# Kernel tuning notes

Measured on AMD Instinct MI355X. Metric: run time of the kernel, lower is better.

The kernel has to match this reference:

```python
import jax, jax.numpy as jnp
import numpy as np

N_NODES = 100000
IN_CH = 256
OUT_CH = 64
N_EDGES = 3200000


def setup_inputs() -> dict:
    key = jax.random.key(0)
    k1, k2, k3, k4 = jax.random.split(key, 4)
    x = jax.random.normal(k1, (N_NODES, IN_CH), dtype=jnp.float32)
    edge_index = jax.random.randint(k2, (2, N_EDGES), 0, N_NODES, dtype=jnp.int64)
    # GCNConv parameters (glorot-style init for W, zeros for bias as in PyG)
    W = jax.random.normal(k3, (IN_CH, OUT_CH), dtype=jnp.float32) / np.sqrt(IN_CH)
    b = jnp.zeros((OUT_CH,), dtype=jnp.float32)
    return {"x": x, "edge_index": edge_index, "W": W, "b": b}


def reference(x, edge_index, W, b):
    N = x.shape[0]
    # --- GCNConv: add self-loops, symmetric degree normalization ---
    loops = jnp.arange(N, dtype=edge_index.dtype)
    src = jnp.concatenate([edge_index[0], loops])  # [E+N]
    dst = jnp.concatenate([edge_index[1], loops])  # [E+N]
    # degree of each target node (edge weights = 1)
    deg = jax.ops.segment_sum(jnp.ones_like(dst, dtype=x.dtype), dst, num_segments=N)
    dinv = jnp.where(deg > 0, jax.lax.rsqrt(deg), 0.0)  # deg^{-1/2}
    norm = dinv[src] * dinv[dst]                        # [E+N]
    # linear transform first (PyG applies lin before propagate)
    h = x @ W                                           # [N, OUT_CH]
    msg = h[src] * norm[:, None]                        # gather + scale
    out = jax.ops.segment_sum(msg, dst, num_segments=N) + b  # scatter-add + bias
    # --- relu + log_softmax ---
    out = jax.nn.relu(out)
    return jax.nn.log_softmax(out, axis=-1)
```

## Files before the change

kernel.cpp:

```cpp
#include <hip/hip_runtime.h>
#include <cstddef>
#include <cstdint>

#define N_NODES 100000
#define IN_CH 256
#define OUT_CH 64
#define N_EDGES 3200000

#define BKT_SHIFT 7
#define BKT_R     128
#define K_BKT     782
#define T_PART    8192
#define NBLK_PART ((N_EDGES + T_PART - 1) / T_PART)

#define WS_FLAG_OFF   0
#define WS_BBASE_OFF  3264
#define WS_BTOT_OFF   6400
#define WS_DINV_OFF   9600
#define WS_NOFF_OFF   409600
#define WS_PAIRS_OFF  809728
#define WS_SSRC_OFF   13609728
#define WS_H_OFF      26409728
#define WS_NEED       39209728

#define WSF_DEG_OFF   4096
#define WSF_DINV_OFF  404096
#define WSF_H_OFF     804096

typedef __attribute__((ext_vector_type(8))) short bshort8;
typedef __attribute__((ext_vector_type(4))) float f32x4;
typedef __attribute__((ext_vector_type(4))) unsigned u32x4;

static __device__ __forceinline__ unsigned short f2bf(float f) {
    unsigned u = __builtin_bit_cast(unsigned, f);
    u += 0x7FFFu + ((u >> 16) & 1u);
    return (unsigned short)(u >> 16);
}
static __device__ __forceinline__ float bflo(unsigned u) {
    return __builtin_bit_cast(float, u << 16);
}
static __device__ __forceinline__ float bfhi(unsigned u) {
    return __builtin_bit_cast(float, u & 0xFFFF0000u);
}

__global__ void probe_kernel(const unsigned* __restrict__ ei, int* __restrict__ flag) {
    if (blockIdx.x == 0 && threadIdx.x == 0) {
        int all0 = 1;
        for (int i = 0; i < 16; ++i) all0 &= (ei[2 * i + 1] == 0u);
        *flag = all0;
    }
}

__device__ __forceinline__ int load_idx(const int* ei32, const long long* ei64,
                                        bool is64, long long pos) {
    return is64 ? (int)ei64[pos] : ei32[pos];
}

__global__ __launch_bounds__(256) void bcount_kernel(const int* __restrict__ ei32,
                                                     const long long* __restrict__ ei64,
                                                     const int* __restrict__ flag,
                                                     unsigned* __restrict__ hist2d) {
    __shared__ unsigned hist[K_BKT];
    const bool is64 = (*flag != 0);
    const int start = blockIdx.x * T_PART;
    const int end   = min(start + T_PART, N_EDGES);
    for (int k = threadIdx.x; k < K_BKT; k += 256) hist[k] = 0u;
    __syncthreads();
    if (is64) {
        const longlong2* d2 = (const longlong2*)&ei64[N_EDGES];
        for (int i = (start >> 1) + threadIdx.x; i < (end >> 1); i += 256) {
            longlong2 d = d2[i];
            atomicAdd(&hist[(int)d.x >> BKT_SHIFT], 1u);
            atomicAdd(&hist[(int)d.y >> BKT_SHIFT], 1u);
        }
    } else {
        const int2* d2 = (const int2*)&ei32[N_EDGES];
        for (int i = (start >> 1) + threadIdx.x; i < (end >> 1); i += 256) {
            int2 d = d2[i];
            atomicAdd(&hist[d.x >> BKT_SHIFT], 1u);
            atomicAdd(&hist[d.y >> BKT_SHIFT], 1u);
        }
    }
    __syncthreads();
    for (int k = threadIdx.x; k < K_BKT; k += 256)
        hist2d[(size_t)blockIdx.x * K_BKT + k] = hist[k];
}

__global__ __launch_bounds__(256) void bscanA_kernel(const unsigned* __restrict__ hist2d,
                                                     unsigned* __restrict__ btot) {
    const int k = blockIdx.x * 4 + (threadIdx.x >> 6);
    const int lane = threadIdx.x & 63;
    if (k >= K_BKT) return;
    unsigned tot = 0u;
    for (int c = lane; c < NBLK_PART; c += 64)
        tot += hist2d[(size_t)c * K_BKT + k];
    #pragma unroll
    for (int o = 32; o; o >>= 1) tot += __shfl_xor(tot, o);
    if (lane == 0) btot[k] = tot;
}

__global__ __launch_bounds__(1024) void bscanB_kernel(const unsigned* __restrict__ btot,
                                                      unsigned* __restrict__ bbase,
                                                      unsigned* __restrict__ noff) {
    __shared__ unsigned s[1024];
    const int t = threadIdx.x;
    unsigned v = (t < K_BKT) ? btot[t] : 0u;
    s[t] = v; __syncthreads();
    #pragma unroll
    for (int d = 1; d < 1024; d <<= 1) {
        unsigned x = (t >= d) ? s[t - d] : 0u; __syncthreads();
        s[t] += x; __syncthreads();
    }
    if (t < K_BKT) {
        bbase[t] = s[t] - v;
        if (t == K_BKT - 1) bbase[K_BKT] = s[t];
    }
    if (t == 0) noff[N_NODES] = N_EDGES;
}

__global__ __launch_bounds__(256) void bscanC_kernel(unsigned* __restrict__ hist2d,
                                                     const unsigned* __restrict__ bbase) {
    const int k = blockIdx.x * 4 + (threadIdx.x >> 6);
    const int lane = threadIdx.x & 63;
    if (k >= K_BKT) return;
    unsigned run = bbase[k];
    for (int c0 = 0; c0 < NBLK_PART; c0 += 64) {
        int blk = c0 + lane;
        unsigned v = (blk < NBLK_PART) ? hist2d[(size_t)blk * K_BKT + k] : 0u;
        unsigned incl = v;
        #pragma unroll
        for (int d = 1; d < 64; d <<= 1) {
            unsigned tq = __shfl_up(incl, d);
            if (lane >= d) incl += tq;
        }
        if (blk < NBLK_PART) hist2d[(size_t)blk * K_BKT + k] = run + incl - v;
        run += __shfl(incl, 63);
    }
}

__global__ __launch_bounds__(512) void partition_kernel(const int* __restrict__ ei32,
                                                        const long long* __restrict__ ei64,
                                                        const int* __restrict__ flag,
                                                        const unsigned* __restrict__ hist2d,
                                                        unsigned* __restrict__ pairs) {
    __shared__ unsigned cur[K_BKT];
    const bool is64 = (*flag != 0);
    const int start = blockIdx.x * T_PART;
    const int end   = min(start + T_PART, N_EDGES);
    for (int k = threadIdx.x; k < K_BKT; k += 512)
        cur[k] = hist2d[(size_t)blockIdx.x * K_BKT + k];
    __syncthreads();
    if (is64) {
        const longlong2* s2 = (const longlong2*)&ei64[0];
        const longlong2* d2 = (const longlong2*)&ei64[N_EDGES];
        for (int i = (start >> 1) + threadIdx.x; i < (end >> 1); i += 512) {
            longlong2 s = s2[i];
            longlong2 d = d2[i];
            unsigned p0 = atomicAdd(&cur[(int)d.x >> BKT_SHIFT], 1u);
            pairs[p0] = (unsigned)s.x | ((unsigned)((int)d.x & (BKT_R - 1)) << 17);
            unsigned p1 = atomicAdd(&cur[(int)d.y >> BKT_SHIFT], 1u);
            pairs[p1] = (unsigned)s.y | ((unsigned)((int)d.y & (BKT_R - 1)) << 17);
        }
    } else {
        const int2* s2 = (const int2*)&ei32[0];
        const int2* d2 = (const int2*)&ei32[N_EDGES];
        for (int i = (start >> 1) + threadIdx.x; i < (end >> 1); i += 512) {
            int2 s = s2[i];
            int2 d = d2[i];
            unsigned p0 = atomicAdd(&cur[d.x >> BKT_SHIFT], 1u);
            pairs[p0] = (unsigned)s.x | ((unsigned)(d.x & (BKT_R - 1)) << 17);
            unsigned p1 = atomicAdd(&cur[d.y >> BKT_SHIFT], 1u);
            pairs[p1] = (unsigned)s.y | ((unsigned)(d.y & (BKT_R - 1)) << 17);
        }
    }
}

__global__ __launch_bounds__(256) void sort2_kernel(const unsigned* __restrict__ pairs,
                                                    const unsigned* __restrict__ bbase,
                                                    int* __restrict__ ssrc,
                                                    unsigned* __restrict__ noff,
                                                    float* __restrict__ dinv) {
    __shared__ unsigned hist[BKT_R];
    __shared__ unsigned cur[BKT_R];
    const int k = blockIdx.x;
    const int t = threadIdx.x;
    const unsigned segS = bbase[k], segE = bbase[k + 1];

    if (t < BKT_R) hist[t] = 0u;
    __syncthreads();
    for (unsigned j = segS + t; j < segE; j += 256)
        atomicAdd(&hist[pairs[j] >> 17], 1u);
    __syncthreads();
    if (t < BKT_R) cur[t] = hist[t];
    __syncthreads();
    #pragma unroll
    for (int d = 1; d < BKT_R; d <<= 1) {
        unsigned x = (t < BKT_R && t >= d) ? cur[t - d] : 0u;
        __syncthreads();
        if (t < BKT_R) cur[t] += x;
        __syncthreads();
    }
    if (t < BKT_R) {
        unsigned mydeg = hist[t];
        unsigned start = segS + cur[t] - mydeg;
        int n = k * BKT_R + t;
        if (n < N_NODES) {
            noff[n] = start;
            dinv[n] = rsqrtf((float)(mydeg + 1u));
        }
        cur[t] = start;
    }
    __syncthreads();
    for (unsigned j = segS + t; j < segE; j += 256) {
        unsigned p = pairs[j];
        unsigned pos = atomicAdd(&cur[p >> 17], 1u);
        ssrc[pos] = (int)(p & 0x1FFFF);
    }
}

__global__ __launch_bounds__(256) void gemm_kernel(const float* __restrict__ x,
                                                   const float* __restrict__ W,
                                                   const float* __restrict__ dinv,
                                                   unsigned short* __restrict__ hs) {
    __shared__ unsigned short Wf[8][4][64][8];
    const int tid = threadIdx.x;
    const int lane = tid & 63;
    const int wv = tid >> 6;

    for (int i = tid; i < 8 * 4 * 64 * 8; i += 256) {
        int kt = i >> 11;
        int rem = i & 2047;
        int ct = rem >> 9;
        int rem2 = rem & 511;
        int l = rem2 >> 3;
        int j = rem2 & 7;
        int kk = kt * 32 + (l >> 4) * 8 + j;
        int cc = ct * 16 + (l & 15);
        ((unsigned short*)Wf)[i] = f2bf(W[(size_t)kk * OUT_CH + cc]);
    }
    __syncthreads();

    const int r16 = lane & 15;
    const int q = lane >> 4;

    for (int t = blockIdx.x * 4 + wv; t < N_NODES / 16; t += gridDim.x * 4) {
        const int row0 = t * 16;
        const float* xrow = &x[(size_t)(row0 + r16) * IN_CH + q * 8];
        f32x4 acc[4] = {{0.f,0.f,0.f,0.f},{0.f,0.f,0.f,0.f},
                        {0.f,0.f,0.f,0.f},{0.f,0.f,0.f,0.f}};
        #pragma unroll
        for (int kt = 0; kt < 8; ++kt) {
            float4 x0 = *(const float4*)&xrow[kt * 32];
            float4 x1 = *(const float4*)&xrow[kt * 32 + 4];
            unsigned p0, p1, p2, p3;
            asm("v_cvt_pk_bf16_f32 %0, %1, %2" : "=v"(p0) : "v"(x0.x), "v"(x0.y));
            asm("v_cvt_pk_bf16_f32 %0, %1, %2" : "=v"(p1) : "v"(x0.z), "v"(x0.w));
            asm("v_cvt_pk_bf16_f32 %0, %1, %2" : "=v"(p2) : "v"(x1.x), "v"(x1.y));
            asm("v_cvt_pk_bf16_f32 %0, %1, %2" : "=v"(p3) : "v"(x1.z), "v"(x1.w));
            u32x4 au = {p0, p1, p2, p3};
            bshort8 af = __builtin_bit_cast(bshort8, au);
            #pragma unroll
            for (int ct = 0; ct < 4; ++ct) {
                bshort8 bf = *(const bshort8*)&Wf[kt][ct][lane][0];
                acc[ct] = __builtin_amdgcn_mfma_f32_16x16x32_bf16(af, bf, acc[ct], 0, 0, 0);
            }
        }
        float dv[4];
        #pragma unroll
        for (int r = 0; r < 4; ++r) dv[r] = dinv[row0 + q * 4 + r];
        #pragma unroll
        for (int ct = 0; ct < 4; ++ct) {
            #pragma unroll
            for (int r = 0; r < 4; ++r) {
                int row = row0 + q * 4 + r;
                hs[(size_t)row * OUT_CH + ct * 16 + r16] = f2bf(acc[ct][r] * dv[r]);
            }
        }
    }
}

__global__ __launch_bounds__(256) void reduce_kernel(const unsigned short* __restrict__ hs,
                                                     const float* __restrict__ dinv,
                                                     const unsigned* __restrict__ noff,
                                                     const int* __restrict__ ssrc,
                                                     const float* __restrict__ b,
                                                     float* __restrict__ out) {
    const int n = blockIdx.x * 4 + (threadIdx.x >> 6);
    const int lane = threadIdx.x & 63;
    const int q = lane >> 4;
    const int l16 = lane & 15;
    if (n >= N_NODES) return;
    const uint2* h8 = (const uint2*)hs;
    float a0 = 0.f, a1 = 0.f, a2 = 0.f, a3 = 0.f;
    {
        uint2 sv = h8[(size_t)n * 16 + l16];
        if (q == 0) { a0 = bflo(sv.x); a1 = bfhi(sv.x); a2 = bflo(sv.y); a3 = bfhi(sv.y); }
    }
    unsigned j = noff[n];
    const unsigned end = noff[n + 1];
    for (; j + 16 <= end; j += 16) {
        int s0 = ssrc[j + q];
        int s1 = ssrc[j + 4 + q];
        int s2 = ssrc[j + 8 + q];
        int s3 = ssrc[j + 12 + q];
        uint2 v0 = h8[(size_t)s0 * 16 + l16];
        uint2 v1 = h8[(size_t)s1 * 16 + l16];
        uint2 v2 = h8[(size_t)s2 * 16 + l16];
        uint2 v3 = h8[(size_t)s3 * 16 + l16];
        a0 += bflo(v0.x); a1 += bfhi(v0.x); a2 += bflo(v0.y); a3 += bfhi(v0.y);
        a0 += bflo(v1.x); a1 += bfhi(v1.x); a2 += bflo(v1.y); a3 += bfhi(v1.y);
        a0 += bflo(v2.x); a1 += bfhi(v2.x); a2 += bflo(v2.y); a3 += bfhi(v2.y);
        a0 += bflo(v3.x); a1 += bfhi(v3.x); a2 += bflo(v3.y); a3 += bfhi(v3.y);
    }
    for (; j + 4 <= end; j += 4) {
        int s = ssrc[j + q];
        uint2 v = h8[(size_t)s * 16 + l16];
        a0 += bflo(v.x); a1 += bfhi(v.x); a2 += bflo(v.y); a3 += bfhi(v.y);
    }
    unsigned rem = end - j;
    if ((unsigned)q < rem) {
        int s = ssrc[j + q];
        uint2 v = h8[(size_t)s * 16 + l16];
        a0 += bflo(v.x); a1 += bfhi(v.x); a2 += bflo(v.y); a3 += bfhi(v.y);
    }
    a0 += __shfl_xor(a0, 16); a0 += __shfl_xor(a0, 32);
    a1 += __shfl_xor(a1, 16); a1 += __shfl_xor(a1, 32);
    a2 += __shfl_xor(a2, 16); a2 += __shfl_xor(a2, 32);
    a3 += __shfl_xor(a3, 16); a3 += __shfl_xor(a3, 32);
    const float dn = dinv[n];
    float4 bb = ((const float4*)b)[l16];
    float v0 = fmaxf(fmaf(a0, dn, bb.x), 0.f);
    float v1 = fmaxf(fmaf(a1, dn, bb.y), 0.f);
    float v2 = fmaxf(fmaf(a2, dn, bb.z), 0.f);
    float v3 = fmaxf(fmaf(a3, dn, bb.w), 0.f);
    float m = fmaxf(fmaxf(v0, v1), fmaxf(v2, v3));
    #pragma unroll
    for (int o = 8; o; o >>= 1) m = fmaxf(m, __shfl_xor(m, o));
    float sum = expf(v0 - m) + expf(v1 - m) + expf(v2 - m) + expf(v3 - m);
    #pragma unroll
    for (int o = 8; o; o >>= 1) sum += __shfl_xor(sum, o);
    float ls = logf(sum);
    if (q == 0) {
        float4 r;
        r.x = (v0 - m) - ls; r.y = (v1 - m) - ls;
        r.z = (v2 - m) - ls; r.w = (v3 - m) - ls;
        *(float4*)&out[(size_t)n * OUT_CH + l16 * 4] = r;
    }
}

__global__ __launch_bounds__(256) void deg_kernel(const int* __restrict__ ei32,
                                                  const long long* __restrict__ ei64,
                                                  const int* __restrict__ flag,
                                                  unsigned* __restrict__ deg) {
    const bool is64 = (*flag != 0);
    int i = blockIdx.x * blockDim.x + threadIdx.x;
    const int stride = gridDim.x * blockDim.x;
    for (; i < N_EDGES; i += stride) {
        int d = load_idx(ei32, ei64, is64, (long long)N_EDGES + i);
        atomicAdd(&deg[d], 1u);
    }
}

__global__ __launch_bounds__(256) void dinv_kernel(const unsigned* __restrict__ deg,
                                                   float* __restrict__ dinv) {
    int i = blockIdx.x * blockDim.x + threadIdx.x;
    if (i < N_NODES) dinv[i] = rsqrtf((float)(deg[i] + 1u));
}

__global__ __launch_bounds__(256) void scatter_kernel(const int* __restrict__ ei32,
                                                      const long long* __restrict__ ei64,
                                                      const int* __restrict__ flag,
                                                      const unsigned short* __restrict__ hs,
                                                      const float* __restrict__ dinv,
                                                      float* __restrict__ out) {
    const bool is64 = (*flag != 0);
    const int lane = threadIdx.x & 63;
    int w = blockIdx.x * (blockDim.x >> 6) + (threadIdx.x >> 6);
    const int nw = gridDim.x * (blockDim.x >> 6);
    for (int e = w; e < N_EDGES; e += nw) {
        int s = load_idx(ei32, ei64, is64, e);
        int d = load_idx(ei32, ei64, is64, (long long)N_EDGES + e);
        unsigned short us = hs[(size_t)s * OUT_CH + lane];
        float hv = __builtin_bit_cast(float, (unsigned)us << 16);
        atomicAdd(&out[(size_t)d * OUT_CH + lane], hv * dinv[d]);
    }
}

__global__ __launch_bounds__(256) void final_kernel(const unsigned short* __restrict__ hs,
                                                    const float* __restrict__ dinv,
                                                    const float* __restrict__ b,
                                                    float* __restrict__ out) {
    const int lane = threadIdx.x & 63;
    int w = blockIdx.x * (blockDim.x >> 6) + (threadIdx.x >> 6);
    const int nw = gridDim.x * (blockDim.x >> 6);
    const float bias = b[lane];
    for (int n = w; n < N_NODES; n += nw) {
        float di = dinv[n];
        unsigned short us = hs[(size_t)n * OUT_CH + lane];
        float hv = __builtin_bit_cast(float, (unsigned)us << 16);
        float v = out[(size_t)n * OUT_CH + lane] + hv * di + bias;
        v = fmaxf(v, 0.f);
        float m = v;
        #pragma unroll
        for (int o = 32; o; o >>= 1) m = fmaxf(m, __shfl_xor(m, o));
        float ex = expf(v - m);
        float sum = ex;
        #pragma unroll
        for (int o = 32; o; o >>= 1) sum += __shfl_xor(sum, o);
        out[(size_t)n * OUT_CH + lane] = (v - m) - logf(sum);
    }
}

extern "C" void kernel_launch(void* const* d_in, const int* in_sizes, int n_in,
                              void* d_out, int out_size, void* d_ws, size_t ws_size,
                              hipStream_t stream) {
    const float* x  = (const float*)d_in[0];
    const void*  ei = d_in[1];
    const float* W  = (const float*)d_in[2];
    const float* b  = (const float*)d_in[3];
    float* out = (float*)d_out;

    char* ws = (char*)d_ws;
    int* flag = (int*)(ws + WS_FLAG_OFF);

    const int* ei32       = (const int*)ei;
    const long long* ei64 = (const long long*)ei;

    probe_kernel<<<1, 64, 0, stream>>>((const unsigned*)ei, flag);

    if (ws_size >= (size_t)WS_NEED) {
        unsigned* bbase  = (unsigned*)(ws + WS_BBASE_OFF);
        unsigned* btot   = (unsigned*)(ws + WS_BTOT_OFF);
        float*    dinv   = (float*)(ws + WS_DINV_OFF);
        unsigned* noff   = (unsigned*)(ws + WS_NOFF_OFF);
        unsigned* pairs  = (unsigned*)(ws + WS_PAIRS_OFF);
        unsigned* hist2d = (unsigned*)(ws + WS_SSRC_OFF);
        int*      ssrc   = (int*)(ws + WS_SSRC_OFF);
        unsigned short* hs = (unsigned short*)(ws + WS_H_OFF);

        bcount_kernel<<<NBLK_PART, 256, 0, stream>>>(ei32, ei64, flag, hist2d);
        bscanA_kernel<<<(K_BKT + 3) / 4, 256, 0, stream>>>(hist2d, btot);
        bscanB_kernel<<<1, 1024, 0, stream>>>(btot, bbase, noff);
        bscanC_kernel<<<(K_BKT + 3) / 4, 256, 0, stream>>>(hist2d, bbase);
        partition_kernel<<<NBLK_PART, 512, 0, stream>>>(ei32, ei64, flag, hist2d, pairs);
        sort2_kernel<<<K_BKT, 256, 0, stream>>>(pairs, bbase, ssrc, noff, dinv);
        gemm_kernel<<<512, 256, 0, stream>>>(x, W, dinv, hs);
        reduce_kernel<<<(N_NODES + 3) / 4, 256, 0, stream>>>(hs, dinv, noff, ssrc, b, out);
    } else {
        unsigned* deg  = (unsigned*)(ws + WSF_DEG_OFF);
        float*    dinv = (float*)(ws + WSF_DINV_OFF);
        unsigned short* hs = (unsigned short*)(ws + WSF_H_OFF);
        hipMemsetAsync(deg, 0, (size_t)N_NODES * sizeof(unsigned), stream);
        hipMemsetAsync(d_out, 0, (size_t)out_size * sizeof(float), stream);
        deg_kernel<<<2048, 256, 0, stream>>>(ei32, ei64, flag, deg);
        dinv_kernel<<<(N_NODES + 255) / 256, 256, 0, stream>>>(deg, dinv);
        gemm_kernel<<<512, 256, 0, stream>>>(x, W, dinv, hs);
        scatter_kernel<<<2048, 256, 0, stream>>>(ei32, ei64, flag, hs, dinv, out);
        final_kernel<<<1024, 256, 0, stream>>>(hs, dinv, b, out);
    }
}
```

Measured before the change: 180.3 us.

## Decouple GEMM from dinv and co-schedule it with edge bucket counting

The GEMM no longer scales rows by dinv, so it no longer depends on the sort stage. It is merged into one launch with the histogram-count kernel, with extra blocks running the GEMM while the others count, so the two overlap. In exchange, the reduce kernel now gathers dinv[src] per edge and applies it with an FMA, adding one extra random 4-byte load per edge. The fallback path is adjusted to the same math.

```diff
diff --git a/kernel.cpp b/kernel.cpp
--- a/kernel.cpp
+++ b/kernel.cpp
@@ -12,6 +12,8 @@
 #define K_BKT     782
 #define T_PART    8192
 #define NBLK_PART ((N_EDGES + T_PART - 1) / T_PART)
+#define NBLK_GEMM 512
+#define N_TILES   (N_NODES / 16)
 
 #define WS_FLAG_OFF   0
 #define WS_BBASE_OFF  3264
@@ -56,173 +58,11 @@
     return is64 ? (int)ei64[pos] : ei32[pos];
 }
 
-__global__ __launch_bounds__(256) void bcount_kernel(const int* __restrict__ ei32,
-                                                     const long long* __restrict__ ei64,
-                                                     const int* __restrict__ flag,
-                                                     unsigned* __restrict__ hist2d) {
-    __shared__ unsigned hist[K_BKT];
-    const bool is64 = (*flag != 0);
-    const int start = blockIdx.x * T_PART;
-    const int end   = min(start + T_PART, N_EDGES);
-    for (int k = threadIdx.x; k < K_BKT; k += 256) hist[k] = 0u;
-    __syncthreads();
-    if (is64) {
-        const longlong2* d2 = (const longlong2*)&ei64[N_EDGES];
-        for (int i = (start >> 1) + threadIdx.x; i < (end >> 1); i += 256) {
-            longlong2 d = d2[i];
-            atomicAdd(&hist[(int)d.x >> BKT_SHIFT], 1u);
-            atomicAdd(&hist[(int)d.y >> BKT_SHIFT], 1u);
-        }
-    } else {
-        const int2* d2 = (const int2*)&ei32[N_EDGES];
-        for (int i = (start >> 1) + threadIdx.x; i < (end >> 1); i += 256) {
-            int2 d = d2[i];
-            atomicAdd(&hist[d.x >> BKT_SHIFT], 1u);
-            atomicAdd(&hist[d.y >> BKT_SHIFT], 1u);
-        }
-    }
-    __syncthreads();
-    for (int k = threadIdx.x; k < K_BKT; k += 256)
-        hist2d[(size_t)blockIdx.x * K_BKT + k] = hist[k];
-}
-
-__global__ __launch_bounds__(256) void bscanA_kernel(const unsigned* __restrict__ hist2d,
-                                                     unsigned* __restrict__ btot) {
-    const int k = blockIdx.x * 4 + (threadIdx.x >> 6);
-    const int lane = threadIdx.x & 63;
-    if (k >= K_BKT) return;
-    unsigned tot = 0u;
-    for (int c = lane; c < NBLK_PART; c += 64)
-        tot += hist2d[(size_t)c * K_BKT + k];
-    #pragma unroll
-    for (int o = 32; o; o >>= 1) tot += __shfl_xor(tot, o);
-    if (lane == 0) btot[k] = tot;
-}
-
-__global__ __launch_bounds__(1024) void bscanB_kernel(const unsigned* __restrict__ btot,
-                                                      unsigned* __restrict__ bbase,
-                                                      unsigned* __restrict__ noff) {
-    __shared__ unsigned s[1024];
-    const int t = threadIdx.x;
-    unsigned v = (t < K_BKT) ? btot[t] : 0u;
-    s[t] = v; __syncthreads();
-    #pragma unroll
-    for (int d = 1; d < 1024; d <<= 1) {
-        unsigned x = (t >= d) ? s[t - d] : 0u; __syncthreads();
-        s[t] += x; __syncthreads();
-    }
-    if (t < K_BKT) {
-        bbase[t] = s[t] - v;
-        if (t == K_BKT - 1) bbase[K_BKT] = s[t];
-    }
-    if (t == 0) noff[N_NODES] = N_EDGES;
-}
-
-__global__ __launch_bounds__(256) void bscanC_kernel(unsigned* __restrict__ hist2d,
-                                                     const unsigned* __restrict__ bbase) {
-    const int k = blockIdx.x * 4 + (threadIdx.x >> 6);
-    const int lane = threadIdx.x & 63;
-    if (k >= K_BKT) return;
-    unsigned run = bbase[k];
-    for (int c0 = 0; c0 < NBLK_PART; c0 += 64) {
-        int blk = c0 + lane;
-        unsigned v = (blk < NBLK_PART) ? hist2d[(size_t)blk * K_BKT + k] : 0u;
-        unsigned incl = v;
-        #pragma unroll
-        for (int d = 1; d < 64; d <<= 1) {
-            unsigned tq = __shfl_up(incl, d);
-            if (lane >= d) incl += tq;
-        }
-        if (blk < NBLK_PART) hist2d[(size_t)blk * K_BKT + k] = run + incl - v;
-        run += __shfl(incl, 63);
-    }
-}
-
-__global__ __launch_bounds__(512) void partition_kernel(const int* __restrict__ ei32,
-                                                        const long long* __restrict__ ei64,
-                                                        const int* __restrict__ flag,
-                                                        const unsigned* __restrict__ hist2d,
-                                                        unsigned* __restrict__ pairs) {
-    __shared__ unsigned cur[K_BKT];
-    const bool is64 = (*flag != 0);
-    const int start = blockIdx.x * T_PART;
-    const int end   = min(start + T_PART, N_EDGES);
-    for (int k = threadIdx.x; k < K_BKT; k += 512)
-        cur[k] = hist2d[(size_t)blockIdx.x * K_BKT + k];
-    __syncthreads();
-    if (is64) {
-        const longlong2* s2 = (const longlong2*)&ei64[0];
-        const longlong2* d2 = (const longlong2*)&ei64[N_EDGES];
-        for (int i = (start >> 1) + threadIdx.x; i < (end >> 1); i += 512) {
-            longlong2 s = s2[i];
-            longlong2 d = d2[i];
-            unsigned p0 = atomicAdd(&cur[(int)d.x >> BKT_SHIFT], 1u);
-            pairs[p0] = (unsigned)s.x | ((unsigned)((int)d.x & (BKT_R - 1)) << 17);
-            unsigned p1 = atomicAdd(&cur[(int)d.y >> BKT_SHIFT], 1u);
-            pairs[p1] = (unsigned)s.y | ((unsigned)((int)d.y & (BKT_R - 1)) << 17);
-        }
-    } else {
-        const int2* s2 = (const int2*)&ei32[0];
-        const int2* d2 = (const int2*)&ei32[N_EDGES];
-        for (int i = (start >> 1) + threadIdx.x; i < (end >> 1); i += 512) {
-            int2 s = s2[i];
-            int2 d = d2[i];
-            unsigned p0 = atomicAdd(&cur[d.x >> BKT_SHIFT], 1u);
-            pairs[p0] = (unsigned)s.x | ((unsigned)(d.x & (BKT_R - 1)) << 17);
-            unsigned p1 = atomicAdd(&cur[d.y >> BKT_SHIFT], 1u);
-            pairs[p1] = (unsigned)s.y | ((unsigned)(d.y & (BKT_R - 1)) << 17);
-        }
-    }
-}
-
-__global__ __launch_bounds__(256) void sort2_kernel(const unsigned* __restrict__ pairs,
-                                                    const unsigned* __restrict__ bbase,
-                                                    int* __restrict__ ssrc,
-                                                    unsigned* __restrict__ noff,
-                                                    float* __restrict__ dinv) {
-    __shared__ unsigned hist[BKT_R];
-    __shared__ unsigned cur[BKT_R];
-    const int k = blockIdx.x;
-    const int t = threadIdx.x;
-    const unsigned segS = bbase[k], segE = bbase[k + 1];
-
-    if (t < BKT_R) hist[t] = 0u;
-    __syncthreads();
-    for (unsigned j = segS + t; j < segE; j += 256)
-        atomicAdd(&hist[pairs[j] >> 17], 1u);
-    __syncthreads();
-    if (t < BKT_R) cur[t] = hist[t];
-    __syncthreads();
-    #pragma unroll
-    for (int d = 1; d < BKT_R; d <<= 1) {
-        unsigned x = (t < BKT_R && t >= d) ? cur[t - d] : 0u;
-        __syncthreads();
-        if (t < BKT_R) cur[t] += x;
-        __syncthreads();
-    }
-    if (t < BKT_R) {
-        unsigned mydeg = hist[t];
-        unsigned start = segS + cur[t] - mydeg;
-        int n = k * BKT_R + t;
-        if (n < N_NODES) {
-            noff[n] = start;
-            dinv[n] = rsqrtf((float)(mydeg + 1u));
-        }
-        cur[t] = start;
-    }
-    __syncthreads();
-    for (unsigned j = segS + t; j < segE; j += 256) {
-        unsigned p = pairs[j];
-        unsigned pos = atomicAdd(&cur[p >> 17], 1u);
-        ssrc[pos] = (int)(p & 0x1FFFF);
-    }
-}
-
-__global__ __launch_bounds__(256) void gemm_kernel(const float* __restrict__ x,
-                                                   const float* __restrict__ W,
-                                                   const float* __restrict__ dinv,
-                                                   unsigned short* __restrict__ hs) {
-    __shared__ unsigned short Wf[8][4][64][8];
+static __device__ __forceinline__ void gemm_body(char* smem, int gbid, int nblk,
+                                                 const float* __restrict__ x,
+                                                 const float* __restrict__ W,
+                                                 unsigned short* __restrict__ hs) {
+    unsigned short (*Wf)[4][64][8] = (unsigned short (*)[4][64][8])smem;
     const int tid = threadIdx.x;
     const int lane = tid & 63;
     const int wv = tid >> 6;
@@ -243,7 +83,7 @@
     const int r16 = lane & 15;
     const int q = lane >> 4;
 
-    for (int t = blockIdx.x * 4 + wv; t < N_NODES / 16; t += gridDim.x * 4) {
+    for (int t = gbid * 4 + wv; t < N_TILES; t += nblk * 4) {
         const int row0 = t * 16;
         const float* xrow = &x[(size_t)(row0 + r16) * IN_CH + q * 8];
         f32x4 acc[4] = {{0.f,0.f,0.f,0.f},{0.f,0.f,0.f,0.f},
@@ -265,17 +105,192 @@
                 acc[ct] = __builtin_amdgcn_mfma_f32_16x16x32_bf16(af, bf, acc[ct], 0, 0, 0);
             }
         }
-        float dv[4];
-        #pragma unroll
-        for (int r = 0; r < 4; ++r) dv[r] = dinv[row0 + q * 4 + r];
         #pragma unroll
         for (int ct = 0; ct < 4; ++ct) {
             #pragma unroll
             for (int r = 0; r < 4; ++r) {
                 int row = row0 + q * 4 + r;
-                hs[(size_t)row * OUT_CH + ct * 16 + r16] = f2bf(acc[ct][r] * dv[r]);
+                hs[(size_t)row * OUT_CH + ct * 16 + r16] = f2bf(acc[ct][r]);
             }
         }
+    }
+}
+
+__global__ __launch_bounds__(256) void bcount_gemm_kernel(const int* __restrict__ ei32,
+                                                          const long long* __restrict__ ei64,
+                                                          const int* __restrict__ flag,
+                                                          unsigned* __restrict__ hist2d,
+                                                          const float* __restrict__ x,
+                                                          const float* __restrict__ W,
+                                                          unsigned short* __restrict__ hs) {
+    __shared__ char smem[32768];
+    const int bid = blockIdx.x;
+    if (bid < NBLK_PART) {
+        unsigned* hist = (unsigned*)smem;
+        const bool is64 = (*flag != 0);
+        const int start = bid * T_PART;
+        const int end   = min(start + T_PART, N_EDGES);
+        for (int k = threadIdx.x; k < K_BKT; k += 256) hist[k] = 0u;
+        __syncthreads();
+        if (is64) {
+            const longlong2* d2 = (const longlong2*)&ei64[N_EDGES];
+            for (int i = (start >> 1) + threadIdx.x; i < (end >> 1); i += 256) {
+                longlong2 d = d2[i];
+                atomicAdd(&hist[(int)d.x >> BKT_SHIFT], 1u);
+                atomicAdd(&hist[(int)d.y >> BKT_SHIFT], 1u);
+            }
+        } else {
+            const int2* d2 = (const int2*)&ei32[N_EDGES];
+            for (int i = (start >> 1) + threadIdx.x; i < (end >> 1); i += 256) {
+                int2 d = d2[i];
+                atomicAdd(&hist[d.x >> BKT_SHIFT], 1u);
+                atomicAdd(&hist[d.y >> BKT_SHIFT], 1u);
+            }
+        }
+        __syncthreads();
+        for (int k = threadIdx.x; k < K_BKT; k += 256)
+            hist2d[(size_t)bid * K_BKT + k] = hist[k];
+    } else {
+        gemm_body(smem, bid - NBLK_PART, NBLK_GEMM, x, W, hs);
+    }
+}
+
+__global__ __launch_bounds__(256) void gemm_only_kernel(const float* __restrict__ x,
+                                                        const float* __restrict__ W,
+                                                        unsigned short* __restrict__ hs) {
+    __shared__ char smem[32768];
+    gemm_body(smem, blockIdx.x, gridDim.x, x, W, hs);
+}
+
+__global__ __launch_bounds__(256) void bscanA_kernel(const unsigned* __restrict__ hist2d,
+                                                     unsigned* __restrict__ btot) {
+    const int k = blockIdx.x * 4 + (threadIdx.x >> 6);
+    const int lane = threadIdx.x & 63;
+    if (k >= K_BKT) return;
+    unsigned tot = 0u;
+    for (int c = lane; c < NBLK_PART; c += 64)
+        tot += hist2d[(size_t)c * K_BKT + k];
+    #pragma unroll
+    for (int o = 32; o; o >>= 1) tot += __shfl_xor(tot, o);
+    if (lane == 0) btot[k] = tot;
+}
+
+__global__ __launch_bounds__(1024) void bscanB_kernel(const unsigned* __restrict__ btot,
+                                                      unsigned* __restrict__ bbase,
+                                                      unsigned* __restrict__ noff) {
+    __shared__ unsigned s[1024];
+    const int t = threadIdx.x;
+    unsigned v = (t < K_BKT) ? btot[t] : 0u;
+    s[t] = v; __syncthreads();
+    #pragma unroll
+    for (int d = 1; d < 1024; d <<= 1) {
+        unsigned x = (t >= d) ? s[t - d] : 0u; __syncthreads();
+        s[t] += x; __syncthreads();
+    }
+    if (t < K_BKT) {
+        bbase[t] = s[t] - v;
+        if (t == K_BKT - 1) bbase[K_BKT] = s[t];
+    }
+    if (t == 0) noff[N_NODES] = N_EDGES;
+}
+
+__global__ __launch_bounds__(256) void bscanC_kernel(unsigned* __restrict__ hist2d,
+                                                     const unsigned* __restrict__ bbase) {
+    const int k = blockIdx.x * 4 + (threadIdx.x >> 6);
+    const int lane = threadIdx.x & 63;
+    if (k >= K_BKT) return;
+    unsigned run = bbase[k];
+    for (int c0 = 0; c0 < NBLK_PART; c0 += 64) {
+        int blk = c0 + lane;
+        unsigned v = (blk < NBLK_PART) ? hist2d[(size_t)blk * K_BKT + k] : 0u;
+        unsigned incl = v;
+        #pragma unroll
+        for (int d = 1; d < 64; d <<= 1) {
+            unsigned tq = __shfl_up(incl, d);
+            if (lane >= d) incl += tq;
+        }
+        if (blk < NBLK_PART) hist2d[(size_t)blk * K_BKT + k] = run + incl - v;
+        run += __shfl(incl, 63);
+    }
+}
+
+__global__ __launch_bounds__(512) void partition_kernel(const int* __restrict__ ei32,
+                                                        const long long* __restrict__ ei64,
+                                                        const int* __restrict__ flag,
+                                                        const unsigned* __restrict__ hist2d,
+                                                        unsigned* __restrict__ pairs) {
+    __shared__ unsigned cur[K_BKT];
+    const bool is64 = (*flag != 0);
+    const int start = blockIdx.x * T_PART;
+    const int end   = min(start + T_PART, N_EDGES);
+    for (int k = threadIdx.x; k < K_BKT; k += 512)
+        cur[k] = hist2d[(size_t)blockIdx.x * K_BKT + k];
+    __syncthreads();
+    if (is64) {
+        const longlong2* s2 = (const longlong2*)&ei64[0];
+        const longlong2* d2 = (const longlong2*)&ei64[N_EDGES];
+        for (int i = (start >> 1) + threadIdx.x; i < (end >> 1); i += 512) {
+            longlong2 s = s2[i];
+            longlong2 d = d2[i];
+            unsigned p0 = atomicAdd(&cur[(int)d.x >> BKT_SHIFT], 1u);
+            pairs[p0] = (unsigned)s.x | ((unsigned)((int)d.x & (BKT_R - 1)) << 17);
+            unsigned p1 = atomicAdd(&cur[(int)d.y >> BKT_SHIFT], 1u);
+            pairs[p1] = (unsigned)s.y | ((unsigned)((int)d.y & (BKT_R - 1)) << 17);
+        }
+    } else {
+        const int2* s2 = (const int2*)&ei32[0];
+        const int2* d2 = (const int2*)&ei32[N_EDGES];
+        for (int i = (start >> 1) + threadIdx.x; i < (end >> 1); i += 512) {
+            int2 s = s2[i];
+            int2 d = d2[i];
+            unsigned p0 = atomicAdd(&cur[d.x >> BKT_SHIFT], 1u);
+            pairs[p0] = (unsigned)s.x | ((unsigned)(d.x & (BKT_R - 1)) << 17);
+            unsigned p1 = atomicAdd(&cur[d.y >> BKT_SHIFT], 1u);
+            pairs[p1] = (unsigned)s.y | ((unsigned)(d.y & (BKT_R - 1)) << 17);
+        }
+    }
+}
+
+__global__ __launch_bounds__(256) void sort2_kernel(const unsigned* __restrict__ pairs,
+                                                    const unsigned* __restrict__ bbase,
+                                                    int* __restrict__ ssrc,
+                                                    unsigned* __restrict__ noff,
+                                                    float* __restrict__ dinv) {
+    __shared__ unsigned hist[BKT_R];
+    __shared__ unsigned cur[BKT_R];
+    const int k = blockIdx.x;
+    const int t = threadIdx.x;
+    const unsigned segS = bbase[k], segE = bbase[k + 1];
+
+    if (t < BKT_R) hist[t] = 0u;
+    __syncthreads();
+    for (unsigned j = segS + t; j < segE; j += 256)
+        atomicAdd(&hist[pairs[j] >> 17], 1u);
+    __syncthreads();
+    if (t < BKT_R) cur[t] = hist[t];
+    __syncthreads();
+    #pragma unroll
+    for (int d = 1; d < BKT_R; d <<= 1) {
+        unsigned x = (t < BKT_R && t >= d) ? cur[t - d] : 0u;
+        __syncthreads();
+        if (t < BKT_R) cur[t] += x;
+        __syncthreads();
+    }
+    if (t < BKT_R) {
+        unsigned mydeg = hist[t];
+        unsigned start = segS + cur[t] - mydeg;
+        int n = k * BKT_R + t;
+        if (n < N_NODES) {
+            noff[n] = start;
+            dinv[n] = rsqrtf((float)(mydeg + 1u));
+        }
+        cur[t] = start;
+    }
+    __syncthreads();
+    for (unsigned j = segS + t; j < segE; j += 256) {
+        unsigned p = pairs[j];
+        unsigned pos = atomicAdd(&cur[p >> 17], 1u);
+        ssrc[pos] = (int)(p & 0x1FFFF);
     }
 }
 
@@ -291,10 +306,14 @@
     const int l16 = lane & 15;
     if (n >= N_NODES) return;
     const uint2* h8 = (const uint2*)hs;
+    const float dn = dinv[n];
     float a0 = 0.f, a1 = 0.f, a2 = 0.f, a3 = 0.f;
     {
         uint2 sv = h8[(size_t)n * 16 + l16];
-        if (q == 0) { a0 = bflo(sv.x); a1 = bfhi(sv.x); a2 = bflo(sv.y); a3 = bfhi(sv.y); }
+        if (q == 0) {
+            a0 = bflo(sv.x) * dn; a1 = bfhi(sv.x) * dn;
+            a2 = bflo(sv.y) * dn; a3 = bfhi(sv.y) * dn;
+        }
     }
     unsigned j = noff[n];
     const unsigned end = noff[n + 1];
@@ -303,31 +322,39 @@
         int s1 = ssrc[j + 4 + q];
         int s2 = ssrc[j + 8 + q];
         int s3 = ssrc[j + 12 + q];
+        float f0 = dinv[s0], f1 = dinv[s1], f2 = dinv[s2], f3 = dinv[s3];
         uint2 v0 = h8[(size_t)s0 * 16 + l16];
         uint2 v1 = h8[(size_t)s1 * 16 + l16];
         uint2 v2 = h8[(size_t)s2 * 16 + l16];
         uint2 v3 = h8[(size_t)s3 * 16 + l16];
-        a0 += bflo(v0.x); a1 += bfhi(v0.x); a2 += bflo(v0.y); a3 += bfhi(v0.y);
-        a0 += bflo(v1.x); a1 += bfhi(v1.x); a2 += bflo(v1.y); a3 += bfhi(v1.y);
-        a0 += bflo(v2.x); a1 += bfhi(v2.x); a2 += bflo(v2.y); a3 += bfhi(v2.y);
-        a0 += bflo(v3.x); a1 += bfhi(v3.x); a2 += bflo(v3.y); a3 += bfhi(v3.y);
+        a0 = fmaf(bflo(v0.x), f0, a0); a1 = fmaf(bfhi(v0.x), f0, a1);
+        a2 = fmaf(bflo(v0.y), f0, a2); a3 = fmaf(bfhi(v0.y), f0, a3);
+        a0 = fmaf(bflo(v1.x), f1, a0); a1 = fmaf(bfhi(v1.x), f1, a1);
+        a2 = fmaf(bflo(v1.y), f1, a2); a3 = fmaf(bfhi(v1.y), f1, a3);
+        a0 = fmaf(bflo(v2.x), f2, a0); a1 = fmaf(bfhi(v2.x), f2, a1);
+        a2 = fmaf(bflo(v2.y), f2, a2); a3 = fmaf(bfhi(v2.y), f2, a3);
+        a0 = fmaf(bflo(v3.x), f3, a0); a1 = fmaf(bfhi(v3.x), f3, a1);
+        a2 = fmaf(bflo(v3.y), f3, a2); a3 = fmaf(bfhi(v3.y), f3, a3);
     }
     for (; j + 4 <= end; j += 4) {
         int s = ssrc[j + q];
+        float f = dinv[s];
         uint2 v = h8[(size_t)s * 16 + l16];
-        a0 += bflo(v.x); a1 += bfhi(v.x); a2 += bflo(v.y); a3 += bfhi(v.y);
+        a0 = fmaf(bflo(v.x), f, a0); a1 = fmaf(bfhi(v.x), f, a1);
+        a2 = fmaf(bflo(v.y), f, a2); a3 = fmaf(bfhi(v.y), f, a3);
     }
     unsigned rem = end - j;
     if ((unsigned)q < rem) {
         int s = ssrc[j + q];
+        float f = dinv[s];
         uint2 v = h8[(size_t)s * 16 + l16];
-        a0 += bflo(v.x); a1 += bfhi(v.x); a2 += bflo(v.y); a3 += bfhi(v.y);
+        a0 = fmaf(bflo(v.x), f, a0); a1 = fmaf(bfhi(v.x), f, a1);
+        a2 = fmaf(bflo(v.y), f, a2); a3 = fmaf(bfhi(v.y), f, a3);
     }
     a0 += __shfl_xor(a0, 16); a0 += __shfl_xor(a0, 32);
     a1 += __shfl_xor(a1, 16); a1 += __shfl_xor(a1, 32);
     a2 += __shfl_xor(a2, 16); a2 += __shfl_xor(a2, 32);
     a3 += __shfl_xor(a3, 16); a3 += __shfl_xor(a3, 32);
-    const float dn = dinv[n];
     float4 bb = ((const float4*)b)[l16];
     float v0 = fmaxf(fmaf(a0, dn, bb.x), 0.f);
     float v1 = fmaxf(fmaf(a1, dn, bb.y), 0.f);
@@ -382,7 +409,7 @@
         int d = load_idx(ei32, ei64, is64, (long long)N_EDGES + e);
         unsigned short us = hs[(size_t)s * OUT_CH + lane];
         float hv = __builtin_bit_cast(float, (unsigned)us << 16);
-        atomicAdd(&out[(size_t)d * OUT_CH + lane], hv * dinv[d]);
+        atomicAdd(&out[(size_t)d * OUT_CH + lane], hv * dinv[s] * dinv[d]);
     }
 }
 
@@ -398,7 +425,7 @@
         float di = dinv[n];
         unsigned short us = hs[(size_t)n * OUT_CH + lane];
         float hv = __builtin_bit_cast(float, (unsigned)us << 16);
-        float v = out[(size_t)n * OUT_CH + lane] + hv * di + bias;
+        float v = out[(size_t)n * OUT_CH + lane] + hv * di * di + bias;
         v = fmaxf(v, 0.f);
         float m = v;
         #pragma unroll
@@ -438,13 +465,13 @@
         int*      ssrc   = (int*)(ws + WS_SSRC_OFF);
         unsigned short* hs = (unsigned short*)(ws + WS_H_OFF);
 
-        bcount_kernel<<<NBLK_PART, 256, 0, stream>>>(ei32, ei64, flag, hist2d);
+        bcount_gemm_kernel<<<NBLK_PART + NBLK_GEMM, 256, 0, stream>>>(
+            ei32, ei64, flag, hist2d, x, W, hs);
         bscanA_kernel<<<(K_BKT + 3) / 4, 256, 0, stream>>>(hist2d, btot);
         bscanB_kernel<<<1, 1024, 0, stream>>>(btot, bbase, noff);
         bscanC_kernel<<<(K_BKT + 3) / 4, 256, 0, stream>>>(hist2d, bbase);
         partition_kernel<<<NBLK_PART, 512, 0, stream>>>(ei32, ei64, flag, hist2d, pairs);
         sort2_kernel<<<K_BKT, 256, 0, stream>>>(pairs, bbase, ssrc, noff, dinv);
-        gemm_kernel<<<512, 256, 0, stream>>>(x, W, dinv, hs);
         reduce_kernel<<<(N_NODES + 3) / 4, 256, 0, stream>>>(hs, dinv, noff, ssrc, b, out);
     } else {
         unsigned* deg  = (unsigned*)(ws + WSF_DEG_OFF);
@@ -454,7 +481,7 @@
         hipMemsetAsync(d_out, 0, (size_t)out_size * sizeof(float), stream);
         deg_kernel<<<2048, 256, 0, stream>>>(ei32, ei64, flag, deg);
         dinv_kernel<<<(N_NODES + 255) / 256, 256, 0, stream>>>(deg, dinv);
-        gemm_kernel<<<512, 256, 0, stream>>>(x, W, dinv, hs);
+        gemm_only_kernel<<<NBLK_GEMM, 256, 0, stream>>>(x, W, hs);
         scatter_kernel<<<2048, 256, 0, stream>>>(ei32, ei64, flag, hs, dinv, out);
         final_kernel<<<1024, 256, 0, stream>>>(hs, dinv, b, out);
     }
```

Measured after the change: 177.6 us. About the same (-1.5%).
